# Kernel optimization log

Measured on AMD Instinct MI355X. Metric: run time of the kernel, lower is better.

The kernel has to match this reference:

```python
import jax, jax.numpy as jnp
import numpy as np

NEG_SLOPE = 0.2
EPS = 1e-16


def gat_layer(x, src, dst, W, a_src, a_dst, b, heads, out_dim, concat):
    """PyG-style GATConv (eval mode, self-loops already included in src/dst)."""
    N = x.shape[0]
    h = (x @ W).reshape(N, heads, out_dim)                 # [N, H, D]
    alpha_src = jnp.einsum('nhd,hd->nh', h, a_src)         # [N, H]
    alpha_dst = jnp.einsum('nhd,hd->nh', h, a_dst)         # [N, H]
    e = alpha_src[src] + alpha_dst[dst]                    # [E, H]
    e = jax.nn.leaky_relu(e, NEG_SLOPE)
    # segment softmax over incoming edges of each dst node
    m = jax.ops.segment_max(e, dst, num_segments=N)        # [N, H]
    e = jnp.exp(e - m[dst])
    denom = jax.ops.segment_sum(e, dst, num_segments=N)    # [N, H]
    alpha = e / (denom[dst] + EPS)                         # [E, H]
    msgs = alpha[:, :, None] * h[src]                      # [E, H, D]
    out = jax.ops.segment_sum(msgs, dst, num_segments=N)   # [N, H, D]
    if concat:
        out = out.reshape(N, heads * out_dim)
    else:
        out = out.mean(axis=1)
    return out + b


def setup_inputs() -> dict:
    key = jax.random.key(0)
    ks = jax.random.split(key, 12)
    N, E, F_IN, C = 100000, 3200000, 512, 64
    H1, D1 = 8, 8
    x = jax.random.normal(ks[0], (N, F_IN), dtype=jnp.float32)
    edge_index = jax.random.randint(ks[1], (2, E), 0, N, dtype=jnp.int64)
    W1 = jax.random.normal(ks[2], (F_IN, H1 * D1), dtype=jnp.float32) / np.sqrt(F_IN)
    a_src1 = jax.random.normal(ks[3], (H1, D1), dtype=jnp.float32) / np.sqrt(D1)
    a_dst1 = jax.random.normal(ks[4], (H1, D1), dtype=jnp.float32) / np.sqrt(D1)
    b1 = jnp.zeros((H1 * D1,), dtype=jnp.float32)
    W2 = jax.random.normal(ks[5], (H1 * D1, C), dtype=jnp.float32) / np.sqrt(H1 * D1)
    a_src2 = jax.random.normal(ks[6], (1, C), dtype=jnp.float32) / np.sqrt(C)
    a_dst2 = jax.random.normal(ks[7], (1, C), dtype=jnp.float32) / np.sqrt(C)
    b2 = jnp.zeros((C,), dtype=jnp.float32)
    return {"x": x, "edge_index": edge_index, "W1": W1, "a_src1": a_src1,
            "a_dst1": a_dst1, "b1": b1, "W2": W2, "a_src2": a_src2,
            "a_dst2": a_dst2, "b2": b2}


def reference(x, edge_index, W1, a_src1, a_dst1, b1, W2, a_src2, a_dst2, b2):
    N = x.shape[0]
    # PyG GATConv adds self loops by default
    loops = jnp.arange(N, dtype=edge_index.dtype)
    src = jnp.concatenate([edge_index[0], loops])
    dst = jnp.concatenate([edge_index[1], loops])
    # eval mode: dropout is identity
    h = gat_layer(x, src, dst, W1, a_src1, a_dst1, b1, heads=8, out_dim=8, concat=True)
    h = jax.nn.elu(h)
    out = gat_layer(h, src, dst, W2, a_src2, a_dst2, b2, heads=1, out_dim=W2.shape[1], concat=False)
    return jax.nn.log_softmax(out, axis=-1)
```

## Files before the change

kernel.cpp:

```cpp
#include <hip/hip_runtime.h>

#define NEG_SLOPE 0.2f
#define NB_SHIFT 8
#define LOG2E 1.4426950408889634f

typedef __attribute__((ext_vector_type(8))) short bf16x8;
typedef __attribute__((ext_vector_type(4))) float f32x4;

__device__ inline unsigned f2bf(float f) {
    unsigned u = __float_as_uint(f);
    return (u + 0x7fffu + ((u >> 16) & 1u)) >> 16;
}
__device__ inline void bf8up(uint4 u, float* f) {
    f[0] = __uint_as_float(u.x << 16); f[1] = __uint_as_float(u.x & 0xffff0000u);
    f[2] = __uint_as_float(u.y << 16); f[3] = __uint_as_float(u.y & 0xffff0000u);
    f[4] = __uint_as_float(u.z << 16); f[5] = __uint_as_float(u.z & 0xffff0000u);
    f[6] = __uint_as_float(u.w << 16); f[7] = __uint_as_float(u.w & 0xffff0000u);
}
__device__ inline float exp2fast(float x) { return __builtin_amdgcn_exp2f(x); }


__global__ void zero_int_kernel(int* __restrict__ p, int n) {
    int i = blockIdx.x * blockDim.x + threadIdx.x;
    if (i < n) p[i] = 0;
}

__global__ __launch_bounds__(256) void bucket_count_kernel(const int* __restrict__ dst, int E,
                                                           int* __restrict__ bcnt, int NB) {
    __shared__ int cnt[512];
    for (int i = threadIdx.x; i < NB; i += 256) cnt[i] = 0;
    __syncthreads();
    int base = blockIdx.x * 16384;
    for (int k = 0; k < 64; ++k) {
        int i = base + k * 256 + threadIdx.x;
        if (i < E) atomicAdd(&cnt[dst[i] >> NB_SHIFT], 1);
    }
    __syncthreads();
    for (int i = threadIdx.x; i < NB; i += 256)
        if (cnt[i]) atomicAdd(&bcnt[i], cnt[i]);
}

__global__ __launch_bounds__(512) void scan_bucket_kernel(const int* __restrict__ bcnt, int nb,
                                                          int* __restrict__ bbase,
                                                          int* __restrict__ bcur,
                                                          int* __restrict__ rowptr, int N) {
    int t = threadIdx.x;
    int v = (t < nb) ? bcnt[t] : 0;
    int s = v;
    #pragma unroll
    for (int d = 1; d < 64; d <<= 1) {
        int o = __shfl_up(s, d);
        if ((t & 63) >= d) s += o;
    }
    __shared__ int ws[8];
    if ((t & 63) == 63) ws[t >> 6] = s;
    __syncthreads();
    int wid = t >> 6;
    int woff = 0;
    for (int w = 0; w < 8; ++w) woff += (w < wid) ? ws[w] : 0;
    int excl = s - v + woff;
    if (t < nb) { bbase[t] = excl; bcur[t] = excl; }
    if (t == 511) { bbase[nb] = excl + v; rowptr[N] = excl + v; }
}

__global__ __launch_bounds__(256) void bucket_scatter_kernel(const int* __restrict__ src,
                                                             const int* __restrict__ dst, int E,
                                                             int* __restrict__ bcur,
                                                             uint2* __restrict__ pairs, int NB) {
    __shared__ int cnt[512];
    __shared__ int base_l[512];
    for (int i = threadIdx.x; i < NB; i += 256) cnt[i] = 0;
    __syncthreads();
    int tbase = blockIdx.x * 8192;
    uint2 e[32];
    int rk[32];
    #pragma unroll
    for (int k = 0; k < 32; ++k) {
        int i = tbase + k * 256 + threadIdx.x;
        if (i < E) {
            e[k].x = (unsigned)src[i];
            e[k].y = (unsigned)dst[i];
            rk[k] = atomicAdd(&cnt[e[k].y >> NB_SHIFT], 1);
        } else {
            rk[k] = -1;
        }
    }
    __syncthreads();
    for (int i = threadIdx.x; i < NB; i += 256)
        base_l[i] = cnt[i] ? atomicAdd(&bcur[i], cnt[i]) : 0;
    __syncthreads();
    #pragma unroll
    for (int k = 0; k < 32; ++k)
        if (rk[k] >= 0) pairs[base_l[e[k].y >> NB_SHIFT] + rk[k]] = e[k];
}

__global__ __launch_bounds__(512) void build_csr_kernel(const uint2* __restrict__ pairs,
                                                        const int* __restrict__ bbase,
                                                        int* __restrict__ rowptr,
                                                        int* __restrict__ csr, int N) {
    __shared__ int cnt[256];
    __shared__ int cur[256];
    __shared__ int ws[4];
    int b = blockIdx.x;
    int lo = bbase[b], hi = bbase[b + 1];
    int t = threadIdx.x;
    if (t < 256) cnt[t] = 0;
    __syncthreads();
    for (int j = lo + t; j < hi; j += 512)
        atomicAdd(&cnt[pairs[j].y & 255], 1);
    __syncthreads();
    int v = 0, s = 0;
    if (t < 256) {
        v = cnt[t];
        s = v;
        #pragma unroll
        for (int d = 1; d < 64; d <<= 1) {
            int o = __shfl_up(s, d);
            if ((t & 63) >= d) s += o;
        }
        if ((t & 63) == 63) ws[t >> 6] = s;
    }
    __syncthreads();
    if (t < 256) {
        int wid = t >> 6;
        int woff = 0;
        for (int w2 = 0; w2 < 4; ++w2) woff += (w2 < wid) ? ws[w2] : 0;
        int excl = lo + s - v + woff;
        int node = (b << NB_SHIFT) + t;
        if (node < N) rowptr[node] = excl;
        cur[t] = excl;
    }
    __syncthreads();
    for (int j = lo + t; j < hi; j += 512) {
        uint2 p = pairs[j];
        int pos = atomicAdd(&cur[p.y & 255], 1);
        csr[pos] = (int)p.x;
    }
}


__global__ __launch_bounds__(512) void gemm1_kernel(const float* __restrict__ x,
                                                    const float* __restrict__ W,
                                                    const float* __restrict__ a_src,
                                                    const float* __restrict__ a_dst,
                                                    unsigned short* __restrict__ hb1,
                                                    float* __restrict__ as1,
                                                    float* __restrict__ ad1, int N) {
    __shared__ unsigned short Wl[16 * 4 * 64 * 8];
    int tid = threadIdx.x;
    for (int i = tid; i < 512 * 16; i += 512) {
        int k = i >> 4, c4 = (i & 15) * 4;
        float4 v = *reinterpret_cast<const float4*>(&W[(size_t)k * 64 + c4]);
        int ks = k >> 5, kin = k & 31, g = kin >> 3, j = kin & 7;
        float vv[4] = {v.x, v.y, v.z, v.w};
        #pragma unroll
        for (int c = 0; c < 4; ++c) {
            int col = c4 + c;
            int nt = col >> 4, l16 = col & 15;
            Wl[(((ks * 4 + nt) * 64) + g * 16 + l16) * 8 + j] = (unsigned short)f2bf(vv[c]);
        }
    }
    __syncthreads();
    int wave = tid >> 6, lane = tid & 63;
    int m = lane & 15, g = lane >> 4;
    int row0 = blockIdx.x * 128 + wave * 16;
    int arow = row0 + m;
    bool aval = arow < N;
    const float* xr = x + (size_t)(aval ? arow : 0) * 512;
    float asw[4], adw[4];
    #pragma unroll
    for (int nt = 0; nt < 4; ++nt) {
        asw[nt] = a_src[nt * 16 + m] * LOG2E;
        adw[nt] = a_dst[nt * 16 + m] * LOG2E;
    }
    f32x4 acc[4] = {{0.f,0.f,0.f,0.f},{0.f,0.f,0.f,0.f},{0.f,0.f,0.f,0.f},{0.f,0.f,0.f,0.f}};
    for (int ks = 0; ks < 16; ++ks) {
        int ko = ks * 32 + g * 8;
        float4 u0 = make_float4(0.f, 0.f, 0.f, 0.f), u1 = u0;
        if (aval) {
            u0 = *reinterpret_cast<const float4*>(xr + ko);
            u1 = *reinterpret_cast<const float4*>(xr + ko + 4);
        }
        bf16x8 af;
        af[0] = (short)f2bf(u0.x); af[1] = (short)f2bf(u0.y);
        af[2] = (short)f2bf(u0.z); af[3] = (short)f2bf(u0.w);
        af[4] = (short)f2bf(u1.x); af[5] = (short)f2bf(u1.y);
        af[6] = (short)f2bf(u1.z); af[7] = (short)f2bf(u1.w);
        #pragma unroll
        for (int nt = 0; nt < 4; ++nt) {
            bf16x8 bf = *reinterpret_cast<const bf16x8*>(&Wl[((ks * 4 + nt) * 64 + lane) * 8]);
            acc[nt] = __builtin_amdgcn_mfma_f32_16x16x32_bf16(af, bf, acc[nt], 0, 0, 0);
        }
    }
    #pragma unroll
    for (int r = 0; r < 4; ++r) {
        int orow = row0 + g * 4 + r;
        if (orow < N) {
            #pragma unroll
            for (int nt = 0; nt < 4; ++nt) {
                float dv = acc[nt][r];
                hb1[(size_t)orow * 64 + nt * 16 + m] = (unsigned short)f2bf(dv);
                float pa = dv * asw[nt];
                float pd = dv * adw[nt];
                pa += __shfl_xor(pa, 1); pa += __shfl_xor(pa, 2); pa += __shfl_xor(pa, 4);
                pd += __shfl_xor(pd, 1); pd += __shfl_xor(pd, 2); pd += __shfl_xor(pd, 4);
                if ((m & 7) == 0) {
                    as1[orow * 8 + nt * 2 + (m >> 3)] = pa;
                    ad1[orow * 8 + nt * 2 + (m >> 3)] = pd;
                }
            }
        }
    }
}


__global__ __launch_bounds__(256) void attn1_kernel(
    const unsigned short* __restrict__ hb1, const float* __restrict__ as1,
    const float* __restrict__ ad1, const int* __restrict__ rowptr,
    const int* __restrict__ csr_src, const float* __restrict__ b1,
    float* __restrict__ helu, int N) {
    int wv = threadIdx.x >> 6;
    int lane = threadIdx.x & 63;
    int d = blockIdx.x * 4 + wv;
    if (d >= N) return;
    int beg = rowptr[d];
    int edeg = rowptr[d + 1] - beg;
    int tot = edeg + 1;
    int q8 = lane & 7, g = lane >> 3;
    float adh = ad1[d * 8 + q8];
    float es = as1[d * 8 + q8] + adh;
    es = fmaxf(es, NEG_SLOPE * es);
    const uint4* hb = reinterpret_cast<const uint4*>(hb1);
    float s = 0.f;
    float acc[8] = {0.f,0.f,0.f,0.f,0.f,0.f,0.f,0.f};
    for (int p0 = 0; p0 < tot; p0 += 8) {
        int p = p0 + g;
        int sn = (p < edeg) ? csr_src[beg + p] : d;
        float e = as1[sn * 8 + q8] + adh;
        e = fmaxf(e, NEG_SLOPE * e);
        float w = (p < tot) ? exp2fast(e - es) : 0.f;
        uint4 u = hb[(size_t)sn * 8 + q8];
        float f[8];
        bf8up(u, f);
        s += w;
        #pragma unroll
        for (int j = 0; j < 8; ++j) acc[j] = fmaf(w, f[j], acc[j]);
    }
    #pragma unroll
    for (int mask = 8; mask < 64; mask <<= 1) {
        s += __shfl_xor(s, mask);
        #pragma unroll
        for (int j = 0; j < 8; ++j) acc[j] += __shfl_xor(acc[j], mask);
    }
    if (lane < 8) {
        float inv = 1.f / (s + 1e-16f);
        const float4* b4 = reinterpret_cast<const float4*>(b1 + q8 * 8);
        float4 ba = b4[0], bb = b4[1];
        float o[8];
        o[0] = fmaf(acc[0], inv, ba.x); o[1] = fmaf(acc[1], inv, ba.y);
        o[2] = fmaf(acc[2], inv, ba.z); o[3] = fmaf(acc[3], inv, ba.w);
        o[4] = fmaf(acc[4], inv, bb.x); o[5] = fmaf(acc[5], inv, bb.y);
        o[6] = fmaf(acc[6], inv, bb.z); o[7] = fmaf(acc[7], inv, bb.w);
        #pragma unroll
        for (int j = 0; j < 8; ++j) o[j] = (o[j] > 0.f) ? o[j] : (__expf(o[j]) - 1.f);
        float4 r0, r1;
        r0.x = o[0]; r0.y = o[1]; r0.z = o[2]; r0.w = o[3];
        r1.x = o[4]; r1.y = o[5]; r1.z = o[6]; r1.w = o[7];
        *reinterpret_cast<float4*>(&helu[(size_t)d * 64 + q8 * 8]) = r0;
        *reinterpret_cast<float4*>(&helu[(size_t)d * 64 + q8 * 8 + 4]) = r1;
    }
}


__global__ __launch_bounds__(256) void gemm2_kernel(
    const float* __restrict__ helu, const float* __restrict__ W2,
    const float* __restrict__ a_src2, const float* __restrict__ a_dst2,
    unsigned short* __restrict__ hb2, float* __restrict__ as2, float* __restrict__ ad2, int N) {
    __shared__ float Ws[64 * 64];
    __shared__ float asw[64], adw[64];
    int tid = threadIdx.x;
    for (int i = tid; i < 64 * 64; i += 256) Ws[i] = W2[i];
    if (tid < 64) { asw[tid] = a_src2[tid] * LOG2E; adw[tid] = a_dst2[tid] * LOG2E; }
    __syncthreads();
    int lane = tid & 63, wv = tid >> 6;
    int stride = gridDim.x * 4;
    for (int row = blockIdx.x * 4 + wv; row < N; row += stride) {
        float hv = helu[(size_t)row * 64 + lane];
        float acc = 0.f;
        #pragma unroll
        for (int k = 0; k < 64; ++k) {
            float v = __shfl(hv, k);
            acc += v * Ws[k * 64 + lane];
        }
        hb2[(size_t)row * 64 + lane] = (unsigned short)f2bf(acc);
        float pa = acc * asw[lane];
        float pb = acc * adw[lane];
        #pragma unroll
        for (int mask = 1; mask < 64; mask <<= 1) {
            pa += __shfl_xor(pa, mask);
            pb += __shfl_xor(pb, mask);
        }
        if (lane == 0) { as2[row] = pa; ad2[row] = pb; }
    }
}


__global__ __launch_bounds__(256) void attn2_kernel(
    const unsigned short* __restrict__ hb2, const float* __restrict__ as2,
    const float* __restrict__ ad2, const int* __restrict__ rowptr,
    const int* __restrict__ csr_src, const float* __restrict__ b2,
    float* __restrict__ out, int N) {
    int wv = threadIdx.x >> 6;
    int lane = threadIdx.x & 63;
    int d = blockIdx.x * 4 + wv;
    if (d >= N) return;
    int beg = rowptr[d];
    int edeg = rowptr[d + 1] - beg;
    int tot = edeg + 1;
    int q8 = lane & 7, g = lane >> 3;
    float add = ad2[d];
    float es = as2[d] + add;
    es = fmaxf(es, NEG_SLOPE * es);
    const uint4* hb = reinterpret_cast<const uint4*>(hb2);
    float s = 0.f;
    float acc[8] = {0.f,0.f,0.f,0.f,0.f,0.f,0.f,0.f};
    for (int p0 = 0; p0 < tot; p0 += 8) {
        int p = p0 + g;
        int sn = (p < edeg) ? csr_src[beg + p] : d;
        float e = as2[sn] + add;
        e = fmaxf(e, NEG_SLOPE * e);
        float w = (p < tot) ? exp2fast(e - es) : 0.f;
        uint4 u = hb[(size_t)sn * 8 + q8];
        float f[8];
        bf8up(u, f);
        s += w;
        #pragma unroll
        for (int j = 0; j < 8; ++j) acc[j] = fmaf(w, f[j], acc[j]);
    }
    #pragma unroll
    for (int mask = 8; mask < 64; mask <<= 1) {
        s += __shfl_xor(s, mask);
        #pragma unroll
        for (int j = 0; j < 8; ++j) acc[j] += __shfl_xor(acc[j], mask);
    }
    float inv = 1.f / (s + 1e-16f);
    const float4* b4 = reinterpret_cast<const float4*>(b2 + q8 * 8);
    float4 ba = b4[0], bb = b4[1];
    float o[8];
    o[0] = fmaf(acc[0], inv, ba.x); o[1] = fmaf(acc[1], inv, ba.y);
    o[2] = fmaf(acc[2], inv, ba.z); o[3] = fmaf(acc[3], inv, ba.w);
    o[4] = fmaf(acc[4], inv, bb.x); o[5] = fmaf(acc[5], inv, bb.y);
    o[6] = fmaf(acc[6], inv, bb.z); o[7] = fmaf(acc[7], inv, bb.w);
    float mx = o[0];
    #pragma unroll
    for (int j = 1; j < 8; ++j) mx = fmaxf(mx, o[j]);
    #pragma unroll
    for (int mask = 1; mask < 8; mask <<= 1) mx = fmaxf(mx, __shfl_xor(mx, mask));
    float sm = 0.f;
    #pragma unroll
    for (int j = 0; j < 8; ++j) sm += __expf(o[j] - mx);
    #pragma unroll
    for (int mask = 1; mask < 8; mask <<= 1) sm += __shfl_xor(sm, mask);
    float lse = mx + __logf(sm);
    if (lane < 8) {
        float4 r0, r1;
        r0.x = o[0] - lse; r0.y = o[1] - lse; r0.z = o[2] - lse; r0.w = o[3] - lse;
        r1.x = o[4] - lse; r1.y = o[5] - lse; r1.z = o[6] - lse; r1.w = o[7] - lse;
        *reinterpret_cast<float4*>(&out[(size_t)d * 64 + q8 * 8]) = r0;
        *reinterpret_cast<float4*>(&out[(size_t)d * 64 + q8 * 8 + 4]) = r1;
    }
}


extern "C" void kernel_launch(void* const* d_in, const int* in_sizes, int n_in,
                              void* d_out, int out_size, void* d_ws, size_t ws_size,
                              hipStream_t stream) {
    const float* x      = (const float*)d_in[0];
    const int*   ei     = (const int*)d_in[1];
    const float* W1     = (const float*)d_in[2];
    const float* a_src1 = (const float*)d_in[3];
    const float* a_dst1 = (const float*)d_in[4];
    const float* b1     = (const float*)d_in[5];
    const float* W2     = (const float*)d_in[6];
    const float* a_src2 = (const float*)d_in[7];
    const float* a_dst2 = (const float*)d_in[8];
    const float* b2     = (const float*)d_in[9];

    int N = in_sizes[0] / 512;
    int E = in_sizes[1] / 2;
    const int* src = ei;
    const int* dst = ei + E;
    int NB = (N + 255) >> NB_SHIFT;

    char* w = (char*)d_ws;
    size_t off = 0;
    auto alloc = [&](size_t bytes) -> void* {
        off = (off + 255) & ~(size_t)255;
        void* p = w + off;
        off += bytes;
        return p;
    };
    int* bcnt   = (int*)alloc((size_t)NB * sizeof(int));
    int* rowptr = (int*)alloc((size_t)(N + 1) * sizeof(int));
    int* bbase  = (int*)alloc((size_t)(NB + 1) * sizeof(int));
    int* bcur   = (int*)alloc((size_t)NB * sizeof(int));
    int* csr    = (int*)alloc((size_t)E * sizeof(int));
    unsigned short* hb1 = (unsigned short*)alloc((size_t)N * 64 * sizeof(unsigned short));
    float* as1  = (float*)alloc((size_t)N * 8 * sizeof(float));
    float* ad1  = (float*)alloc((size_t)N * 8 * sizeof(float));
    float* helu = (float*)alloc((size_t)N * 64 * sizeof(float));
    uint2* pairs = (uint2*)helu;
    unsigned short* hb2 = hb1;
    float* as2 = as1;
    float* ad2 = ad1;

    zero_int_kernel<<<(NB + 255) / 256, 256, 0, stream>>>(bcnt, NB);
    bucket_count_kernel<<<(E + 16383) / 16384, 256, 0, stream>>>(dst, E, bcnt, NB);
    scan_bucket_kernel<<<1, 512, 0, stream>>>(bcnt, NB, bbase, bcur, rowptr, N);
    bucket_scatter_kernel<<<(E + 8191) / 8192, 256, 0, stream>>>(src, dst, E, bcur, pairs, NB);
    build_csr_kernel<<<NB, 512, 0, stream>>>(pairs, bbase, rowptr, csr, N);

    gemm1_kernel<<<(N + 127) / 128, 512, 0, stream>>>(x, W1, a_src1, a_dst1, hb1, as1, ad1, N);
    attn1_kernel<<<(N + 3) / 4, 256, 0, stream>>>(hb1, as1, ad1, rowptr, csr, b1, helu, N);

    gemm2_kernel<<<2048, 256, 0, stream>>>(helu, W2, a_src2, a_dst2, hb2, as2, ad2, N);
    attn2_kernel<<<(N + 3) / 4, 256, 0, stream>>>(hb2, as2, ad2, rowptr, csr, b2, (float*)d_out, N);
}
```

Before: 409.4 us.

## Fuse layer-2 GEMM into attn1 epilogue and pack edge pairs into 32 bits

The second-layer 64x64 projection and its attention logits move into the attn1 kernel, so the ELU output stays in registers and no longer makes a round trip through global memory, and the separate gemm2 launch is removed. Each attn1 block now loads W2 (16KB) into shared memory, which adds per-block setup and may lower occupancy. Separately, the bucket sort packs each (src, low 8 bits of dst) pair into one 32-bit word instead of a uint2, halving the traffic for the pairs buffer. The packing assumes src fits in 24 bits, which holds for N=100000.

```diff
diff --git a/kernel.cpp b/kernel.cpp
--- a/kernel.cpp
+++ b/kernel.cpp
@@ -66,21 +66,23 @@
 __global__ __launch_bounds__(256) void bucket_scatter_kernel(const int* __restrict__ src,
                                                              const int* __restrict__ dst, int E,
                                                              int* __restrict__ bcur,
-                                                             uint2* __restrict__ pairs, int NB) {
+                                                             unsigned* __restrict__ pairs, int NB) {
     __shared__ int cnt[512];
     __shared__ int base_l[512];
     for (int i = threadIdx.x; i < NB; i += 256) cnt[i] = 0;
     __syncthreads();
     int tbase = blockIdx.x * 8192;
-    uint2 e[32];
+    unsigned e[32];
+    int bk[32];
     int rk[32];
     #pragma unroll
     for (int k = 0; k < 32; ++k) {
         int i = tbase + k * 256 + threadIdx.x;
         if (i < E) {
-            e[k].x = (unsigned)src[i];
-            e[k].y = (unsigned)dst[i];
-            rk[k] = atomicAdd(&cnt[e[k].y >> NB_SHIFT], 1);
+            int dv = dst[i];
+            e[k] = (unsigned)src[i] | ((unsigned)(dv & 255) << 24);
+            bk[k] = dv >> NB_SHIFT;
+            rk[k] = atomicAdd(&cnt[bk[k]], 1);
         } else {
             rk[k] = -1;
         }
@@ -91,10 +93,10 @@
     __syncthreads();
     #pragma unroll
     for (int k = 0; k < 32; ++k)
-        if (rk[k] >= 0) pairs[base_l[e[k].y >> NB_SHIFT] + rk[k]] = e[k];
-}
-
-__global__ __launch_bounds__(512) void build_csr_kernel(const uint2* __restrict__ pairs,
+        if (rk[k] >= 0) pairs[base_l[bk[k]] + rk[k]] = e[k];
+}
+
+__global__ __launch_bounds__(512) void build_csr_kernel(const unsigned* __restrict__ pairs,
                                                         const int* __restrict__ bbase,
                                                         int* __restrict__ rowptr,
                                                         int* __restrict__ csr, int N) {
@@ -107,7 +109,7 @@
     if (t < 256) cnt[t] = 0;
     __syncthreads();
     for (int j = lo + t; j < hi; j += 512)
-        atomicAdd(&cnt[pairs[j].y & 255], 1);
+        atomicAdd(&cnt[pairs[j] >> 24], 1);
     __syncthreads();
     int v = 0, s = 0;
     if (t < 256) {
@@ -132,9 +134,9 @@
     }
     __syncthreads();
     for (int j = lo + t; j < hi; j += 512) {
-        uint2 p = pairs[j];
-        int pos = atomicAdd(&cur[p.y & 255], 1);
-        csr[pos] = (int)p.x;
+        unsigned p = pairs[j];
+        int pos = atomicAdd(&cur[p >> 24], 1);
+        csr[pos] = (int)(p & 0x00FFFFFFu);
     }
 }
 
@@ -218,9 +220,17 @@
     const unsigned short* __restrict__ hb1, const float* __restrict__ as1,
     const float* __restrict__ ad1, const int* __restrict__ rowptr,
     const int* __restrict__ csr_src, const float* __restrict__ b1,
-    float* __restrict__ helu, int N) {
-    int wv = threadIdx.x >> 6;
-    int lane = threadIdx.x & 63;
+    const float* __restrict__ W2, const float* __restrict__ a_src2,
+    const float* __restrict__ a_dst2, unsigned short* __restrict__ hb2,
+    float* __restrict__ as2, float* __restrict__ ad2, int N) {
+    __shared__ float Ws[64 * 64];
+    __shared__ float asw2[64], adw2[64];
+    int tid = threadIdx.x;
+    for (int i = tid; i < 64 * 64; i += 256) Ws[i] = W2[i];
+    if (tid < 64) { asw2[tid] = a_src2[tid] * LOG2E; adw2[tid] = a_dst2[tid] * LOG2E; }
+    __syncthreads();
+    int wv = tid >> 6;
+    int lane = tid & 63;
     int d = blockIdx.x * 4 + wv;
     if (d >= N) return;
     int beg = rowptr[d];
@@ -252,56 +262,34 @@
         #pragma unroll
         for (int j = 0; j < 8; ++j) acc[j] += __shfl_xor(acc[j], mask);
     }
-    if (lane < 8) {
-        float inv = 1.f / (s + 1e-16f);
-        const float4* b4 = reinterpret_cast<const float4*>(b1 + q8 * 8);
-        float4 ba = b4[0], bb = b4[1];
-        float o[8];
-        o[0] = fmaf(acc[0], inv, ba.x); o[1] = fmaf(acc[1], inv, ba.y);
-        o[2] = fmaf(acc[2], inv, ba.z); o[3] = fmaf(acc[3], inv, ba.w);
-        o[4] = fmaf(acc[4], inv, bb.x); o[5] = fmaf(acc[5], inv, bb.y);
-        o[6] = fmaf(acc[6], inv, bb.z); o[7] = fmaf(acc[7], inv, bb.w);
-        #pragma unroll
-        for (int j = 0; j < 8; ++j) o[j] = (o[j] > 0.f) ? o[j] : (__expf(o[j]) - 1.f);
-        float4 r0, r1;
-        r0.x = o[0]; r0.y = o[1]; r0.z = o[2]; r0.w = o[3];
-        r1.x = o[4]; r1.y = o[5]; r1.z = o[6]; r1.w = o[7];
-        *reinterpret_cast<float4*>(&helu[(size_t)d * 64 + q8 * 8]) = r0;
-        *reinterpret_cast<float4*>(&helu[(size_t)d * 64 + q8 * 8 + 4]) = r1;
-    }
-}
-
-
-__global__ __launch_bounds__(256) void gemm2_kernel(
-    const float* __restrict__ helu, const float* __restrict__ W2,
-    const float* __restrict__ a_src2, const float* __restrict__ a_dst2,
-    unsigned short* __restrict__ hb2, float* __restrict__ as2, float* __restrict__ ad2, int N) {
-    __shared__ float Ws[64 * 64];
-    __shared__ float asw[64], adw[64];
-    int tid = threadIdx.x;
-    for (int i = tid; i < 64 * 64; i += 256) Ws[i] = W2[i];
-    if (tid < 64) { asw[tid] = a_src2[tid] * LOG2E; adw[tid] = a_dst2[tid] * LOG2E; }
-    __syncthreads();
-    int lane = tid & 63, wv = tid >> 6;
-    int stride = gridDim.x * 4;
-    for (int row = blockIdx.x * 4 + wv; row < N; row += stride) {
-        float hv = helu[(size_t)row * 64 + lane];
-        float acc = 0.f;
-        #pragma unroll
-        for (int k = 0; k < 64; ++k) {
-            float v = __shfl(hv, k);
-            acc += v * Ws[k * 64 + lane];
-        }
-        hb2[(size_t)row * 64 + lane] = (unsigned short)f2bf(acc);
-        float pa = acc * asw[lane];
-        float pb = acc * adw[lane];
-        #pragma unroll
-        for (int mask = 1; mask < 64; mask <<= 1) {
-            pa += __shfl_xor(pa, mask);
-            pb += __shfl_xor(pb, mask);
-        }
-        if (lane == 0) { as2[row] = pa; ad2[row] = pb; }
-    }
+    float inv = 1.f / (s + 1e-16f);
+    const float4* b4 = reinterpret_cast<const float4*>(b1 + q8 * 8);
+    float4 ba = b4[0], bb = b4[1];
+    float o[8];
+    o[0] = fmaf(acc[0], inv, ba.x); o[1] = fmaf(acc[1], inv, ba.y);
+    o[2] = fmaf(acc[2], inv, ba.z); o[3] = fmaf(acc[3], inv, ba.w);
+    o[4] = fmaf(acc[4], inv, bb.x); o[5] = fmaf(acc[5], inv, bb.y);
+    o[6] = fmaf(acc[6], inv, bb.z); o[7] = fmaf(acc[7], inv, bb.w);
+    #pragma unroll
+    for (int j = 0; j < 8; ++j) o[j] = (o[j] > 0.f) ? o[j] : (__expf(o[j]) - 1.f);
+    float h2v = 0.f;
+    #pragma unroll
+    for (int c = 0; c < 8; ++c) {
+        #pragma unroll
+        for (int i = 0; i < 8; ++i) {
+            float hv = __shfl(o[i], c);
+            h2v = fmaf(hv, Ws[(c * 8 + i) * 64 + lane], h2v);
+        }
+    }
+    hb2[(size_t)d * 64 + lane] = (unsigned short)f2bf(h2v);
+    float pa = h2v * asw2[lane];
+    float pb = h2v * adw2[lane];
+    #pragma unroll
+    for (int mask = 1; mask < 64; mask <<= 1) {
+        pa += __shfl_xor(pa, mask);
+        pb += __shfl_xor(pb, mask);
+    }
+    if (lane == 0) { as2[d] = pa; ad2[d] = pb; }
 }
 
 
@@ -405,14 +393,13 @@
     int* bbase  = (int*)alloc((size_t)(NB + 1) * sizeof(int));
     int* bcur   = (int*)alloc((size_t)NB * sizeof(int));
     int* csr    = (int*)alloc((size_t)E * sizeof(int));
+    unsigned* pairs = (unsigned*)alloc((size_t)E * sizeof(unsigned));
     unsigned short* hb1 = (unsigned short*)alloc((size_t)N * 64 * sizeof(unsigned short));
     float* as1  = (float*)alloc((size_t)N * 8 * sizeof(float));
     float* ad1  = (float*)alloc((size_t)N * 8 * sizeof(float));
-    float* helu = (float*)alloc((size_t)N * 64 * sizeof(float));
-    uint2* pairs = (uint2*)helu;
-    unsigned short* hb2 = hb1;
-    float* as2 = as1;
-    float* ad2 = ad1;
+    unsigned short* hb2 = (unsigned short*)alloc((size_t)N * 64 * sizeof(unsigned short));
+    float* as2  = (float*)alloc((size_t)N * sizeof(float));
+    float* ad2  = (float*)alloc((size_t)N * sizeof(float));
 
     zero_int_kernel<<<(NB + 255) / 256, 256, 0, stream>>>(bcnt, NB);
     bucket_count_kernel<<<(E + 16383) / 16384, 256, 0, stream>>>(dst, E, bcnt, NB);
@@ -421,8 +408,7 @@
     build_csr_kernel<<<NB, 512, 0, stream>>>(pairs, bbase, rowptr, csr, N);
 
     gemm1_kernel<<<(N + 127) / 128, 512, 0, stream>>>(x, W1, a_src1, a_dst1, hb1, as1, ad1, N);
-    attn1_kernel<<<(N + 3) / 4, 256, 0, stream>>>(hb1, as1, ad1, rowptr, csr, b1, helu, N);
-
-    gemm2_kernel<<<2048, 256, 0, stream>>>(helu, W2, a_src2, a_dst2, hb2, as2, ad2, N);
+    attn1_kernel<<<(N + 3) / 4, 256, 0, stream>>>(hb1, as1, ad1, rowptr, csr, b1,
+                                                  W2, a_src2, a_dst2, hb2, as2, ad2, N);
     attn2_kernel<<<(N + 3) / 4, 256, 0, stream>>>(hb2, as2, ad2, rowptr, csr, b2, (float*)d_out, N);
 }
```

Result: no change. 412.7 us (+0.8%).
